# Optimization experiments

Measured on AMD Instinct MI355X. Metric: run time of the kernel, lower is better.

The kernel has to match this reference:

```python
import jax, jax.numpy as jnp
import numpy as np

D_MODEL, D_STATE, HEAD_DIM, EXPAND, K, N_GROUPS = 1024, 128, 64, 2, 4, 1
D_INNER = EXPAND * D_MODEL            # 2048
N_HEADS = D_INNER // HEAD_DIM         # 32
D_PROJ = 2 * D_INNER + 2 * N_GROUPS * D_STATE + N_HEADS  # 4384
EPS = 1e-6


def setup_inputs() -> dict:
    key = jax.random.key(0)
    ks = jax.random.split(key, 8)
    B, L = 2, 2048
    x = jax.random.normal(ks[0], (B, L, D_MODEL), dtype=jnp.float32)
    norm_w = jnp.ones((D_MODEL,), jnp.float32)
    in_proj_w = jax.random.normal(ks[1], (D_PROJ, D_MODEL), jnp.float32) * (D_MODEL ** -0.5)
    conv_w = jax.random.normal(ks[2], (D_INNER, 1, K), jnp.float32) * (K ** -0.5)
    conv_b = jnp.zeros((D_INNER,), jnp.float32)
    A_log = jnp.log(jax.random.uniform(ks[3], (N_HEADS,)) * 15.0 + 1.0)
    D = jnp.ones((N_HEADS,), jnp.float32)
    dt_bias = jnp.log(jax.random.uniform(ks[4], (N_HEADS,)) * 0.099 + 0.001)
    out_proj_w = jax.random.normal(ks[5], (D_MODEL, D_INNER), jnp.float32) * (D_INNER ** -0.5)
    return {"x": x, "norm_w": norm_w, "in_proj_w": in_proj_w, "conv_w": conv_w,
            "conv_b": conv_b, "A_log": A_log, "D": D, "dt_bias": dt_bias,
            "out_proj_w": out_proj_w}


def _silu(v):
    return v * jax.nn.sigmoid(v)


def reference(x, norm_w, in_proj_w, conv_w, conv_b, A_log, D, dt_bias, out_proj_w):
    Bsz, L, _ = x.shape
    residual = x
    # RMSNorm (pre-norm)
    xn = x * jax.lax.rsqrt(jnp.mean(x * x, axis=-1, keepdims=True) + EPS) * norm_w
    proj = xn @ in_proj_w.T                                     # (B, L, D_PROJ)
    # split fused projection -> (z, x_ssm, B, C, dt_raw)
    i = 0
    z = proj[..., i:i + D_INNER]; i += D_INNER
    x_ssm = proj[..., i:i + D_INNER]; i += D_INNER
    bc = N_GROUPS * D_STATE
    Bm = proj[..., i:i + bc].reshape(Bsz, L, N_GROUPS, D_STATE); i += bc
    Cm = proj[..., i:i + bc].reshape(Bsz, L, N_GROUPS, D_STATE); i += bc
    dt_raw = proj[..., i:i + N_HEADS]
    # causal depthwise conv1d (torch pad=K-1 then slice [:L] == left-pad K-1)
    xc = jnp.transpose(x_ssm, (0, 2, 1))                        # (B, D_INNER, L)
    xc = jax.lax.conv_general_dilated(
        xc, conv_w, window_strides=(1,), padding=[(K - 1, 0)],
        dimension_numbers=("NCH", "OIH", "NCH"), feature_group_count=D_INNER)
    xc = xc + conv_b[None, :, None]
    x_conv = _silu(jnp.transpose(xc, (0, 2, 1)))                # (B, L, D_INNER)
    # discretisation
    dt = jax.nn.softplus(dt_raw + dt_bias)                      # (B, L, H)
    dA = jnp.exp(-jnp.exp(A_log)[None, None, :] * dt)           # (B, L, H)
    x_heads = x_conv.reshape(Bsz, L, N_HEADS, HEAD_DIM)
    dt_x = dt[..., None] * x_heads                              # (B, L, H, P)
    group_idx = jnp.arange(N_HEADS) // (N_HEADS // N_GROUPS)
    Bg = Bm[:, :, group_idx, :]                                 # (B, L, H, N)
    Cg = Cm[:, :, group_idx, :]
    # sequential selective scan over time via lax.scan (fp32 state)
    def step(h, inp):
        dA_t, dtx_t, B_t, C_t = inp                             # (B,H),(B,H,P),(B,H,N),(B,H,N)
        h = h * dA_t[..., None, None] + dtx_t[..., None] * B_t[:, :, None, :]
        y_t = jnp.einsum("bhpn,bhn->bhp", h, C_t)
        return h, y_t
    h0 = jnp.zeros((Bsz, N_HEADS, HEAD_DIM, D_STATE), jnp.float32)
    xs = (jnp.moveaxis(dA, 1, 0).astype(jnp.float32),
          jnp.moveaxis(dt_x, 1, 0).astype(jnp.float32),
          jnp.moveaxis(Bg, 1, 0).astype(jnp.float32),
          jnp.moveaxis(Cg, 1, 0).astype(jnp.float32))
    _, y = jax.lax.scan(step, h0, xs)                           # y: (L, B, H, P)
    y = jnp.moveaxis(y, 0, 1).astype(x.dtype)                   # (B, L, H, P)
    y = y + D[None, None, :, None] * x_heads
    y = y.reshape(Bsz, L, D_INNER) * _silu(z)                   # gated output
    return residual + y @ out_proj_w.T
```

## Files before the change

kernel.cpp:

```cpp
#include <hip/hip_runtime.h>
#include <math.h>

#define B_SZ     2
#define L_SEQ    2048
#define DM       1024
#define DP       4384
#define PS       4480
#define DI       2048
#define NH       32
#define HD       64
#define DS       128
#define M_ROWS   (B_SZ * L_SEQ)
#define QCH      64
#define NC       (L_SEQ / QCH)

typedef __bf16 bf16x8 __attribute__((ext_vector_type(8)));
typedef __bf16 bf16x4 __attribute__((ext_vector_type(4)));
typedef __bf16 bf16x2 __attribute__((ext_vector_type(2)));
typedef float  f32x4  __attribute__((ext_vector_type(4)));

__device__ __forceinline__ void gload16(const void* g, void* l) {
    __builtin_amdgcn_global_load_lds(
        (const __attribute__((address_space(1))) unsigned int*)g,
        (__attribute__((address_space(3))) unsigned int*)l,
        16, 0, 0);
}

__global__ __launch_bounds__(256) void k_prep(const float* __restrict__ Wp,
                                              __bf16* __restrict__ Wpb,
                                              const float* __restrict__ x,
                                              const float* __restrict__ w,
                                              __bf16* __restrict__ xn) {
    int tid = threadIdx.x;
    if (blockIdx.x < 4384) {
        int i = blockIdx.x * 256 + tid;
        float4 v = ((const float4*)Wp)[i];
        bf16x4 o = { (__bf16)v.x, (__bf16)v.y, (__bf16)v.z, (__bf16)v.w };
        ((bf16x4*)Wpb)[i] = o;
        return;
    }
    int row = blockIdx.x - 4384;
    const float4* x4 = (const float4*)(x + (long)row * DM);
    float4 v = x4[tid];
    float ss = v.x * v.x + v.y * v.y + v.z * v.z + v.w * v.w;
    #pragma unroll
    for (int off = 32; off > 0; off >>= 1) ss += __shfl_xor(ss, off, 64);
    __shared__ float sred[4];
    if ((tid & 63) == 0) sred[tid >> 6] = ss;
    __syncthreads();
    float tot = sred[0] + sred[1] + sred[2] + sred[3];
    float scale = rsqrtf(tot * (1.0f / (float)DM) + 1e-6f);
    const float4* w4 = (const float4*)w;
    float4 wv = w4[tid];
    bf16x4 o = { (__bf16)(v.x * scale * wv.x), (__bf16)(v.y * scale * wv.y),
                 (__bf16)(v.z * scale * wv.z), (__bf16)(v.w * scale * wv.w) };
    ((bf16x4*)(xn + (long)row * DM))[tid] = o;
}

__global__ __launch_bounds__(256) void k_gemm_bf(const __bf16* __restrict__ A,
                                                 const __bf16* __restrict__ W,
                                                 __bf16* __restrict__ Cb,
                                                 float* __restrict__ Dt,
                                                 int Nw, int K, int ldc) {
    __shared__ __align__(16) __bf16 As[2][128 * 64];
    __shared__ __align__(16) __bf16 Bs[2][128 * 64];
    int t = threadIdx.x;

    int gx = gridDim.x;
    int nwg = gx * gridDim.y;
    int orig = blockIdx.y * gx + blockIdx.x;
    int wgid = (nwg & 7) ? orig : ((orig & 7) * (nwg >> 3) + (orig >> 3));
    int bx = wgid % gx, by = wgid / gx;
    int bm = by * 128, bn = bx * 128;

    int lane = t & 63, w = t >> 6;

    int rl = lane >> 3;
    int lc = (lane & 7) ^ rl;
    int rbase = w * 32 + rl;
    const __bf16* Agp[4];
    const __bf16* Wgp[4];
    #pragma unroll
    for (int i = 0; i < 4; i++) {
        Agp[i] = A + (long)(bm + rbase + i * 8) * K + lc * 8;
        int rb = bn + rbase + i * 8; if (rb >= Nw) rb = Nw - 1;
        Wgp[i] = W + (long)rb * K + lc * 8;
    }

    int wm = (w & 1) * 64, wn = (w >> 1) * 64;
    int ln = lane & 15;
    int q  = lane >> 4;

    f32x4 acc[4][4] = {};

    int nst = K >> 6;

    #pragma unroll
    for (int i = 0; i < 4; i++) {
        gload16(Agp[i], As[0] + (w * 4 + i) * 512);
        gload16(Wgp[i], Bs[0] + (w * 4 + i) * 512);
    }

    int cur = 0;
    for (int s = 0; s < nst; ++s) {
        if (s + 1 < nst) {
            long k1 = (long)(s + 1) << 6;
            #pragma unroll
            for (int i = 0; i < 4; i++) {
                gload16(Agp[i] + k1, As[cur ^ 1] + (w * 4 + i) * 512);
                gload16(Wgp[i] + k1, Bs[cur ^ 1] + (w * 4 + i) * 512);
            }
            asm volatile("s_waitcnt vmcnt(8)" ::: "memory");
        } else {
            asm volatile("s_waitcnt vmcnt(0)" ::: "memory");
        }
        __builtin_amdgcn_sched_barrier(0);
        __builtin_amdgcn_s_barrier();
        __builtin_amdgcn_sched_barrier(0);
        __builtin_amdgcn_s_setprio(1);

        const __bf16* Asc = As[cur];
        const __bf16* Bsc = Bs[cur];
        #pragma unroll
        for (int h = 0; h < 2; h++) {
            int ch = (4 * h + q);
            int koff = ((ch ^ (ln & 7)) << 3);
            bf16x8 af[4], bfr[4];
            #pragma unroll
            for (int i = 0; i < 4; i++)
                af[i]  = *(const bf16x8*)(Asc + (wm + ln + i * 16) * 64 + koff);
            #pragma unroll
            for (int j = 0; j < 4; j++)
                bfr[j] = *(const bf16x8*)(Bsc + (wn + ln + j * 16) * 64 + koff);
            #pragma unroll
            for (int i = 0; i < 4; i++)
                #pragma unroll
                for (int j = 0; j < 4; j++)
                    acc[i][j] = __builtin_amdgcn_mfma_f32_16x16x32_bf16(
                                    af[i], bfr[j], acc[i][j], 0, 0, 0);
        }
        __builtin_amdgcn_s_setprio(0);
        __builtin_amdgcn_sched_barrier(0);
        __builtin_amdgcn_s_barrier();
        __builtin_amdgcn_sched_barrier(0);
        cur ^= 1;
    }

    int colbase = bn + wn + ln;
    #pragma unroll
    for (int i = 0; i < 4; i++) {
        #pragma unroll
        for (int r = 0; r < 4; r++) {
            int m = bm + wm + i * 16 + (lane >> 4) * 4 + r;
            long off = (long)m * ldc + colbase;
            #pragma unroll
            for (int j = 0; j < 4; j++) {
                float v = acc[i][j][r];
                Cb[off + j * 16] = (__bf16)v;
                int col = colbase + j * 16;
                if (col >= 4352 && col < 4384)
                    Dt[(long)m * 32 + (col - 4352)] = v;
            }
        }
    }
}

__global__ __launch_bounds__(256) void k_gemm_out(const __bf16* __restrict__ A,
                                                  const __bf16* __restrict__ W,
                                                  const float* __restrict__ resid,
                                                  float* __restrict__ Cf,
                                                  int K, int ldc) {
    __shared__ __align__(16) __bf16 As[2][64 * 64];
    __shared__ __align__(16) __bf16 Bs[2][128 * 64];
    int t = threadIdx.x;

    int gx = gridDim.x;
    int nwg = gx * gridDim.y;
    int orig = blockIdx.y * gx + blockIdx.x;
    int wgid = (nwg & 7) ? orig : ((orig & 7) * (nwg >> 3) + (orig >> 3));
    int bx = wgid % gx, by = wgid / gx;
    int bm = by * 64, bn = bx * 128;

    int lane = t & 63, w = t >> 6;

    int rl = lane >> 3;
    int lc = (lane & 7) ^ rl;
    const __bf16* Agp[2];
    const __bf16* Wgp[4];
    #pragma unroll
    for (int i = 0; i < 2; i++)
        Agp[i] = A + (long)(bm + w * 16 + i * 8 + rl) * K + lc * 8;
    #pragma unroll
    for (int i = 0; i < 4; i++)
        Wgp[i] = W + (long)(bn + w * 32 + i * 8 + rl) * K + lc * 8;

    int wm = (w & 1) * 32, wn = (w >> 1) * 64;
    int ln = lane & 15;
    int q  = lane >> 4;

    f32x4 acc[2][4] = {};

    int nst = K >> 6;

    #pragma unroll
    for (int i = 0; i < 2; i++) gload16(Agp[i], As[0] + (w * 2 + i) * 512);
    #pragma unroll
    for (int i = 0; i < 4; i++) gload16(Wgp[i], Bs[0] + (w * 4 + i) * 512);

    int cur = 0;
    for (int s = 0; s < nst; ++s) {
        if (s + 1 < nst) {
            long k1 = (long)(s + 1) << 6;
            #pragma unroll
            for (int i = 0; i < 2; i++)
                gload16(Agp[i] + k1, As[cur ^ 1] + (w * 2 + i) * 512);
            #pragma unroll
            for (int i = 0; i < 4; i++)
                gload16(Wgp[i] + k1, Bs[cur ^ 1] + (w * 4 + i) * 512);
            asm volatile("s_waitcnt vmcnt(6)" ::: "memory");
        } else {
            asm volatile("s_waitcnt vmcnt(0)" ::: "memory");
        }
        __builtin_amdgcn_sched_barrier(0);
        __builtin_amdgcn_s_barrier();
        __builtin_amdgcn_sched_barrier(0);
        __builtin_amdgcn_s_setprio(1);

        const __bf16* Asc = As[cur];
        const __bf16* Bsc = Bs[cur];
        #pragma unroll
        for (int h = 0; h < 2; h++) {
            int ch = (4 * h + q);
            int koff = ((ch ^ (ln & 7)) << 3);
            bf16x8 af[2], bfr[4];
            #pragma unroll
            for (int i = 0; i < 2; i++)
                af[i]  = *(const bf16x8*)(Asc + (wm + ln + i * 16) * 64 + koff);
            #pragma unroll
            for (int j = 0; j < 4; j++)
                bfr[j] = *(const bf16x8*)(Bsc + (wn + ln + j * 16) * 64 + koff);
            #pragma unroll
            for (int i = 0; i < 2; i++)
                #pragma unroll
                for (int j = 0; j < 4; j++)
                    acc[i][j] = __builtin_amdgcn_mfma_f32_16x16x32_bf16(
                                    af[i], bfr[j], acc[i][j], 0, 0, 0);
        }
        __builtin_amdgcn_s_setprio(0);
        __builtin_amdgcn_sched_barrier(0);
        __builtin_amdgcn_s_barrier();
        __builtin_amdgcn_sched_barrier(0);
        cur ^= 1;
    }

    int colbase = bn + wn + ln;
    #pragma unroll
    for (int i = 0; i < 2; i++) {
        #pragma unroll
        for (int r = 0; r < 4; r++) {
            int m = bm + wm + i * 16 + (lane >> 4) * 4 + r;
            long off = (long)m * ldc + colbase;
            #pragma unroll
            for (int j = 0; j < 4; j++) {
                float v = acc[i][j][r] + resid[off + j * 16];
                Cf[off + j * 16] = v;
            }
        }
    }
}

__global__ __launch_bounds__(256) void k_chunk(const __bf16* __restrict__ projb,
                                               const float* __restrict__ dtraw,
                                               const float* __restrict__ cw,
                                               const float* __restrict__ cb,
                                               const float* __restrict__ A_log,
                                               const float* __restrict__ dt_bias,
                                               const float* __restrict__ Dv,
                                               float* __restrict__ clog,
                                               __bf16* __restrict__ yssm,
                                               __bf16* __restrict__ Sloc) {
    int blk = blockIdx.x;
    int c  = blk & 31;
    int hh = (blk >> 5) & 31;
    int b  = blk >> 10;
    int tid = threadIdx.x;
    long rowbase = (long)b * L_SEQ + c * QCH;

    __shared__ __align__(16) __bf16 sB[64 * 136];
    __shared__ __align__(16) __bf16 sU[128 * 72];
    __shared__ __align__(16) __bf16 sXT[64 * 72];
    __shared__ __align__(16) __bf16 sXCM[67 * 72];
    __shared__ __align__(16) __bf16 sXCo[64 * 72];
    __shared__ float sCW[256];
    __shared__ float sCB[64];
    __shared__ float sclog[64];
    __shared__ float sdt[64];
    __shared__ float sw[64];

    #pragma unroll
    for (int j = 0; j < 4; j++) {
        int off = j * 256 + tid;
        int t  = off >> 4;
        int n8 = (off & 15) * 8;
        const __bf16* pr = projb + (rowbase + t) * (long)PS;
        *(bf16x8*)&sB[t * 136 + n8] = *(const bf16x8*)(pr + 4096 + n8);
        *(bf16x8*)&sU[t * 136 + n8] = *(const bf16x8*)(pr + 4224 + n8);
    }
    #pragma unroll
    for (int j = 0; j < 3; j++) {
        int off = j * 256 + tid;
        if (off < 536) {
            int ss = off >> 3;
            int p8 = (off & 7) * 8;
            bf16x8 xv;
            #pragma unroll
            for (int k = 0; k < 8; k++) xv[k] = (__bf16)0.0f;
            if (c > 0 || ss >= 3)
                xv = *(const bf16x8*)(projb + (rowbase + ss - 3) * (long)PS + DI + hh * HD + p8);
            *(bf16x8*)&sXCM[ss * 72 + p8] = xv;
        }
    }
    sCW[tid] = cw[hh * 256 + tid];
    if (tid < 64) sCB[tid] = cb[hh * 64 + tid];

    if (tid < 64) {
        float xr = dtraw[(rowbase + tid) * 32 + hh] + dt_bias[hh];
        float dt = (xr > 20.0f) ? xr : log1pf(expf(xr));
        float la = -expf(A_log[hh]);
        float v = la * dt;
        #pragma unroll
        for (int off = 1; off < 64; off <<= 1) {
            float u = __shfl_up(v, off, 64);
            if (tid >= off) v += u;
        }
        sdt[tid] = dt;
        sclog[tid] = v;
        clog[(rowbase + tid) * NH + hh] = v;
    }
    __syncthreads();

    {
        int p8 = (tid & 7) * 8;
        float wreg[8][4], breg[8];
        #pragma unroll
        for (int e = 0; e < 8; e++) {
            breg[e] = sCB[p8 + e];
            #pragma unroll
            for (int j = 0; j < 4; j++) wreg[e][j] = sCW[(p8 + e) * 4 + j];
        }
        #pragma unroll
        for (int i = 0; i < 2; i++) {
            int s = i * 32 + (tid >> 3);
            bf16x8 r0 = *(const bf16x8*)&sXCM[(s + 0) * 72 + p8];
            bf16x8 r1 = *(const bf16x8*)&sXCM[(s + 1) * 72 + p8];
            bf16x8 r2 = *(const bf16x8*)&sXCM[(s + 2) * 72 + p8];
            bf16x8 r3 = *(const bf16x8*)&sXCM[(s + 3) * 72 + p8];
            float dts = sdt[s];
            bf16x8 oc;
            #pragma unroll
            for (int e = 0; e < 8; e++) {
                float acc = breg[e];
                acc = fmaf(wreg[e][0], (float)r0[e], acc);
                acc = fmaf(wreg[e][1], (float)r1[e], acc);
                acc = fmaf(wreg[e][2], (float)r2[e], acc);
                acc = fmaf(wreg[e][3], (float)r3[e], acc);
                float xc = acc / (1.0f + expf(-acc));
                oc[e] = (__bf16)xc;
                sXT[(p8 + e) * 72 + s] = (__bf16)(dts * xc);
            }
            *(bf16x8*)&sXCo[s * 72 + p8] = oc;
        }
    }
    if (tid < 64) sw[tid] = expf(sclog[63] - sclog[tid]);
    __syncthreads();

    int lane = tid & 63, w = tid >> 6;
    int ln = lane & 15;
    int quad = lane >> 4;
    int kc = quad * 8;

    bf16x8 caf[4];
    #pragma unroll
    for (int k0 = 0; k0 < 4; k0++)
        caf[k0] = *(const bf16x8*)&sU[(16 * w + ln) * 136 + kc + k0 * 32];
    f32x4 g[4] = {};
    #pragma unroll
    for (int j = 0; j < 4; j++)
        #pragma unroll
        for (int k0 = 0; k0 < 4; k0++) {
            bf16x8 bf_ = *(const bf16x8*)&sB[(16 * j + ln) * 136 + kc + k0 * 32];
            g[j] = __builtin_amdgcn_mfma_f32_16x16x32_bf16(caf[k0], bf_, g[j], 0, 0, 0);
        }

    {
        int trow = 16 * w + quad * 4;
        #pragma unroll
        for (int r = 0; r < 4; r++) {
            int t = trow + r;
            float ct = sclog[t];
            #pragma unroll
            for (int j = 0; j < 4; j++) {
                int s = 16 * j + ln;
                float v = (s <= t) ? g[j][r] * expf(ct - sclog[s]) : 0.0f;
                sXCM[t * 72 + s] = (__bf16)v;
            }
        }
    }
    __syncthreads();

    #pragma unroll
    for (int j = 0; j < 4; j++) {
        int s  = tid & 63;
        int n8 = (j * 4 + (tid >> 6)) * 8;
        bf16x8 v = *(const bf16x8*)&sB[s * 136 + n8];
        #pragma unroll
        for (int k = 0; k < 8; k++) sU[(n8 + k) * 72 + s] = v[k];
    }

    {
        float Dh = Dv[hh];
        bf16x8 maf[2];
        #pragma unroll
        for (int k0 = 0; k0 < 2; k0++)
            maf[k0] = *(const bf16x8*)&sXCM[(16 * w + ln) * 72 + kc + k0 * 32];
        f32x4 y[4] = {};
        #pragma unroll
        for (int j = 0; j < 4; j++)
            #pragma unroll
            for (int k0 = 0; k0 < 2; k0++) {
                bf16x8 xf = *(const bf16x8*)&sXT[(16 * j + ln) * 72 + kc + k0 * 32];
                y[j] = __builtin_amdgcn_mfma_f32_16x16x32_bf16(maf[k0], xf, y[j], 0, 0, 0);
            }
        #pragma unroll
        for (int j = 0; j < 4; j++)
            #pragma unroll
            for (int r = 0; r < 4; r++) {
                int t = 16 * w + quad * 4 + r;
                int p = 16 * j + ln;
                float v = y[j][r] + Dh * (float)sXCo[t * 72 + p];
                yssm[(rowbase + t) * DI + hh * HD + p] = (__bf16)v;
            }
    }
    __syncthreads();

    {
        bf16x8 xaf[2];
        #pragma unroll
        for (int k0 = 0; k0 < 2; k0++) {
            bf16x8 raw = *(const bf16x8*)&sXT[(16 * w + ln) * 72 + kc + k0 * 32];
            bf16x8 sc;
            #pragma unroll
            for (int jj = 0; jj < 8; jj++) {
                int s = kc + k0 * 32 + jj;
                sc[jj] = (__bf16)((float)raw[jj] * sw[s]);
            }
            xaf[k0] = sc;
        }
        f32x4 sacc[8] = {};
        #pragma unroll
        for (int j = 0; j < 8; j++)
            #pragma unroll
            for (int k0 = 0; k0 < 2; k0++) {
                bf16x8 btf = *(const bf16x8*)&sU[(16 * j + ln) * 72 + kc + k0 * 32];
                sacc[j] = __builtin_amdgcn_mfma_f32_16x16x32_bf16(xaf[k0], btf, sacc[j], 0, 0, 0);
            }
        long sbase = ((long)(b * NH + hh) * NC + c) * (HD * DS);
        #pragma unroll
        for (int j = 0; j < 8; j++)
            #pragma unroll
            for (int r = 0; r < 4; r++) {
                int p = 16 * w + quad * 4 + r;
                int n = 16 * j + ln;
                Sloc[sbase + p * DS + n] = (__bf16)sacc[j][r];
            }
    }
}

__global__ __launch_bounds__(256) void k_carry_f2b(__bf16* __restrict__ Sloc,
                                                   const float* __restrict__ clog,
                                                   const float* __restrict__ Wo,
                                                   __bf16* __restrict__ Wob) {
    int bid = blockIdx.x;
    int tid = threadIdx.x;
    if (bid >= 1024) {
        int i = (bid - 1024) * 256 + tid;
        float4 v = ((const float4*)Wo)[i];
        bf16x4 o = { (__bf16)v.x, (__bf16)v.y, (__bf16)v.z, (__bf16)v.w };
        ((bf16x4*)Wob)[i] = o;
        return;
    }
    int idx = bid * 256 + tid;
    int n2 = idx & 63;
    int p  = (idx >> 6) & 63;
    int hh = (idx >> 12) & 31;
    int b  = idx >> 17;
    long base = ((long)(b * NH + hh) * NC) * (HD * DS) + p * DS + n2 * 2;
    float T0 = 0.0f, T1 = 0.0f;
    for (int c = 0; c < NC; c++) {
        float lam = expf(clog[((long)b * L_SEQ + c * QCH + QCH - 1) * NH + hh]);
        long a = base + (long)c * (HD * DS);
        bf16x2 Sv = *(const bf16x2*)&Sloc[a];
        float S0 = (float)Sv[0], S1 = (float)Sv[1];
        bf16x2 Tv = { (__bf16)T0, (__bf16)T1 };
        *(bf16x2*)&Sloc[a] = Tv;
        T0 = fmaf(T0, lam, S0);
        T1 = fmaf(T1, lam, S1);
    }
}

__global__ __launch_bounds__(256, 2) void k_fix(const __bf16* __restrict__ projb,
                                                const __bf16* __restrict__ Sloc,
                                                const float* __restrict__ clog,
                                                const __bf16* __restrict__ yb,
                                                __bf16* __restrict__ yg) {
    int blk = blockIdx.x;
    int c  = blk & 31;
    int hh = (blk >> 5) & 31;
    int b  = blk >> 10;

    __shared__ __align__(16) __bf16 sC[64 * 136];
    __shared__ __align__(16) __bf16 sH[64 * 136];
    __shared__ float sP[64];

    int tid = threadIdx.x;
    long hbase = ((long)(b * NH + hh) * NC + c) * (HD * DS);
    long rowbase = (long)b * L_SEQ + c * QCH;

    #pragma unroll
    for (int j = 0; j < 4; j++) {
        int off = j * 256 + tid;
        int t  = off >> 4;
        int n8 = (off & 15) * 8;
        *(bf16x8*)&sC[t * 136 + n8] =
            *(const bf16x8*)(projb + (rowbase + t) * (long)PS + 4224 + n8);
    }
    #pragma unroll
    for (int j = 0; j < 4; j++) {
        int off = j * 256 + tid;
        int p  = off >> 4;
        int n8 = (off & 15) * 8;
        *(bf16x8*)&sH[p * 136 + n8] = *(const bf16x8*)&Sloc[hbase + (long)off * 8];
    }
    if (tid < 64) sP[tid] = expf(clog[(rowbase + tid) * NH + hh]);
    __syncthreads();

    int lane = tid & 63, w = tid >> 6;
    int ln = lane & 15;
    int quad = lane >> 4;
    int kc = quad * 8;

    bf16x8 caf[4];
    #pragma unroll
    for (int k0 = 0; k0 < 4; k0++)
        caf[k0] = *(const bf16x8*)&sC[(16 * w + ln) * 136 + kc + k0 * 32];
    f32x4 acc4[4] = {};
    #pragma unroll
    for (int j = 0; j < 4; j++)
        #pragma unroll
        for (int k0 = 0; k0 < 4; k0++) {
            bf16x8 hf = *(const bf16x8*)&sH[(16 * j + ln) * 136 + kc + k0 * 32];
            acc4[j] = __builtin_amdgcn_mfma_f32_16x16x32_bf16(caf[k0], hf, acc4[j], 0, 0, 0);
        }

    #pragma unroll
    for (int j = 0; j < 4; j++)
        #pragma unroll
        for (int r = 0; r < 4; r++) {
            int t = 16 * w + quad * 4 + r;
            int p = 16 * j + ln;
            long row = rowbase + t;
            long yoff = row * DI + hh * HD + p;
            float pm = sP[t];
            float z = (float)projb[row * (long)PS + hh * HD + p];
            float o = ((float)yb[yoff] + pm * acc4[j][r]) * (z / (1.0f + expf(-z)));
            yg[yoff] = (__bf16)o;
        }
}

extern "C" void kernel_launch(void* const* d_in, const int* in_sizes, int n_in,
                              void* d_out, int out_size, void* d_ws, size_t ws_size,
                              hipStream_t stream) {
    const float* x       = (const float*)d_in[0];
    const float* norm_w  = (const float*)d_in[1];
    const float* Wp      = (const float*)d_in[2];
    const float* cw      = (const float*)d_in[3];
    const float* cb      = (const float*)d_in[4];
    const float* A_log   = (const float*)d_in[5];
    const float* Dv      = (const float*)d_in[6];
    const float* dt_bias = (const float*)d_in[7];
    const float* Wo      = (const float*)d_in[8];
    float* out = (float*)d_out;

    float* ws     = (float*)d_ws;
    __bf16* projb = (__bf16*)ws;
    float* dtraw  = ws    + 9175040;
    float* clog   = dtraw + 131072;
    float* ybh    = clog  + 131072;
    float* ybf    = ybh   + 4194304;
    float* wob_s  = ybf   + 4194304;
    float* U      = wob_s + 1048576;

    __bf16* xnb  = (__bf16*)U;
    __bf16* Wpb  = (__bf16*)(U + 2097152);
    __bf16* Sloc = (__bf16*)U;
    __bf16* Wob  = (__bf16*)wob_s;
    __bf16* ybb  = (__bf16*)ybf;
    __bf16* yb   = (__bf16*)ybh;

    k_prep<<<4384 + M_ROWS, 256, 0, stream>>>(Wp, Wpb, x, norm_w, xnb);
    {
        dim3 g(PS / 128, M_ROWS / 128);
        k_gemm_bf<<<g, 256, 0, stream>>>(xnb, Wpb, projb, dtraw, DP, DM, PS);
    }

    k_chunk<<<B_SZ * NH * NC, 256, 0, stream>>>(projb, dtraw, cw, cb, A_log,
                                                dt_bias, Dv, clog, yb, Sloc);
    k_carry_f2b<<<3072, 256, 0, stream>>>(Sloc, clog, Wo, Wob);
    k_fix<<<B_SZ * NH * NC, 256, 0, stream>>>(projb, Sloc, clog, yb, ybb);

    {
        dim3 g(DM / 128, M_ROWS / 64);
        k_gemm_out<<<g, 256, 0, stream>>>(ybb, Wob, x, out, DI, DM);
    }
}
```

Measured before the change: 261.1 us.

## Restructure input projection GEMM into 256x128 tiles with triple-buffered split prefetch

The input-projection GEMM now uses 512-thread blocks covering 256x128 output tiles, with eight waves in a 4x2 layout. LDS goes from double to triple buffering, loading two stages ahead. Each k-step's global-to-LDS loads are split into two halves interleaved with the two MFMA half-steps. The aim is to hide memory latency better and reuse the weight tile across more rows. In exchange it uses more LDS per block (about 144KB) and launches half as many blocks, which may reduce occupancy and wave coverage on the CUs.

```diff
diff --git a/kernel.cpp b/kernel.cpp
--- a/kernel.cpp
+++ b/kernel.cpp
@@ -57,13 +57,13 @@
     ((bf16x4*)(xn + (long)row * DM))[tid] = o;
 }
 
-__global__ __launch_bounds__(256) void k_gemm_bf(const __bf16* __restrict__ A,
+__global__ __launch_bounds__(512) void k_gemm_in(const __bf16* __restrict__ A,
                                                  const __bf16* __restrict__ W,
                                                  __bf16* __restrict__ Cb,
                                                  float* __restrict__ Dt,
                                                  int Nw, int K, int ldc) {
-    __shared__ __align__(16) __bf16 As[2][128 * 64];
-    __shared__ __align__(16) __bf16 Bs[2][128 * 64];
+    __shared__ __align__(16) __bf16 As[3][256 * 64];
+    __shared__ __align__(16) __bf16 Bs[3][128 * 64];
     int t = threadIdx.x;
 
     int gx = gridDim.x;
@@ -71,23 +71,25 @@
     int orig = blockIdx.y * gx + blockIdx.x;
     int wgid = (nwg & 7) ? orig : ((orig & 7) * (nwg >> 3) + (orig >> 3));
     int bx = wgid % gx, by = wgid / gx;
-    int bm = by * 128, bn = bx * 128;
+    int bm = by * 256, bn = bx * 128;
 
     int lane = t & 63, w = t >> 6;
 
     int rl = lane >> 3;
     int lc = (lane & 7) ^ rl;
-    int rbase = w * 32 + rl;
     const __bf16* Agp[4];
-    const __bf16* Wgp[4];
-    #pragma unroll
-    for (int i = 0; i < 4; i++) {
-        Agp[i] = A + (long)(bm + rbase + i * 8) * K + lc * 8;
-        int rb = bn + rbase + i * 8; if (rb >= Nw) rb = Nw - 1;
+    #pragma unroll
+    for (int i = 0; i < 4; i++)
+        Agp[i] = A + (long)(bm + w * 32 + i * 8 + rl) * K + lc * 8;
+    const __bf16* Wgp[2];
+    #pragma unroll
+    for (int i = 0; i < 2; i++) {
+        int rb = bn + w * 16 + i * 8 + rl; if (rb >= Nw) rb = Nw - 1;
         Wgp[i] = W + (long)rb * K + lc * 8;
     }
 
-    int wm = (w & 1) * 64, wn = (w >> 1) * 64;
+    int wr = w >> 1, wc = w & 1;
+    int wm = wr * 64, wn = wc * 64;
     int ln = lane & 15;
     int q  = lane >> 4;
 
@@ -96,35 +98,35 @@
     int nst = K >> 6;
 
     #pragma unroll
-    for (int i = 0; i < 4; i++) {
-        gload16(Agp[i], As[0] + (w * 4 + i) * 512);
-        gload16(Wgp[i], Bs[0] + (w * 4 + i) * 512);
-    }
+    for (int p = 0; p < 2; ++p) {
+        long kk = (long)p << 6;
+        #pragma unroll
+        for (int i = 0; i < 4; i++) gload16(Agp[i] + kk, As[p] + (w * 4 + i) * 512);
+        #pragma unroll
+        for (int i = 0; i < 2; i++) gload16(Wgp[i] + kk, Bs[p] + (w * 2 + i) * 512);
+    }
+    asm volatile("s_waitcnt vmcnt(6)" ::: "memory");
+    __builtin_amdgcn_sched_barrier(0);
+    __builtin_amdgcn_s_barrier();
+    __builtin_amdgcn_sched_barrier(0);
 
     int cur = 0;
     for (int s = 0; s < nst; ++s) {
-        if (s + 1 < nst) {
-            long k1 = (long)(s + 1) << 6;
-            #pragma unroll
-            for (int i = 0; i < 4; i++) {
-                gload16(Agp[i] + k1, As[cur ^ 1] + (w * 4 + i) * 512);
-                gload16(Wgp[i] + k1, Bs[cur ^ 1] + (w * 4 + i) * 512);
-            }
-            asm volatile("s_waitcnt vmcnt(8)" ::: "memory");
-        } else {
-            asm volatile("s_waitcnt vmcnt(0)" ::: "memory");
-        }
-        __builtin_amdgcn_sched_barrier(0);
-        __builtin_amdgcn_s_barrier();
-        __builtin_amdgcn_sched_barrier(0);
-        __builtin_amdgcn_s_setprio(1);
-
         const __bf16* Asc = As[cur];
         const __bf16* Bsc = Bs[cur];
-        #pragma unroll
-        for (int h = 0; h < 2; h++) {
-            int ch = (4 * h + q);
-            int koff = ((ch ^ (ln & 7)) << 3);
+        int nx2 = cur + 2; if (nx2 >= 3) nx2 -= 3;
+        bool pre = (s + 2 < nst);
+        long k2 = (long)(s + 2) << 6;
+        __bf16* Ad = As[nx2];
+        __bf16* Bd = Bs[nx2];
+
+        if (pre) {
+            gload16(Agp[0] + k2, Ad + (w * 4 + 0) * 512);
+            gload16(Agp[1] + k2, Ad + (w * 4 + 1) * 512);
+            gload16(Agp[2] + k2, Ad + (w * 4 + 2) * 512);
+        }
+        {
+            int koff = ((q ^ (ln & 7)) << 3);
             bf16x8 af[4], bfr[4];
             #pragma unroll
             for (int i = 0; i < 4; i++)
@@ -132,18 +134,49 @@
             #pragma unroll
             for (int j = 0; j < 4; j++)
                 bfr[j] = *(const bf16x8*)(Bsc + (wn + ln + j * 16) * 64 + koff);
+            __builtin_amdgcn_s_setprio(1);
             #pragma unroll
             for (int i = 0; i < 4; i++)
                 #pragma unroll
                 for (int j = 0; j < 4; j++)
                     acc[i][j] = __builtin_amdgcn_mfma_f32_16x16x32_bf16(
                                     af[i], bfr[j], acc[i][j], 0, 0, 0);
-        }
-        __builtin_amdgcn_s_setprio(0);
+            __builtin_amdgcn_s_setprio(0);
+        }
         __builtin_amdgcn_sched_barrier(0);
         __builtin_amdgcn_s_barrier();
         __builtin_amdgcn_sched_barrier(0);
-        cur ^= 1;
+
+        if (pre) {
+            gload16(Agp[3] + k2, Ad + (w * 4 + 3) * 512);
+            gload16(Wgp[0] + k2, Bd + (w * 2 + 0) * 512);
+            gload16(Wgp[1] + k2, Bd + (w * 2 + 1) * 512);
+        }
+        {
+            int koff = (((4 + q) ^ (ln & 7)) << 3);
+            bf16x8 af[4], bfr[4];
+            #pragma unroll
+            for (int i = 0; i < 4; i++)
+                af[i]  = *(const bf16x8*)(Asc + (wm + ln + i * 16) * 64 + koff);
+            #pragma unroll
+            for (int j = 0; j < 4; j++)
+                bfr[j] = *(const bf16x8*)(Bsc + (wn + ln + j * 16) * 64 + koff);
+            __builtin_amdgcn_s_setprio(1);
+            #pragma unroll
+            for (int i = 0; i < 4; i++)
+                #pragma unroll
+                for (int j = 0; j < 4; j++)
+                    acc[i][j] = __builtin_amdgcn_mfma_f32_16x16x32_bf16(
+                                    af[i], bfr[j], acc[i][j], 0, 0, 0);
+            __builtin_amdgcn_s_setprio(0);
+        }
+        if (pre) asm volatile("s_waitcnt vmcnt(6)" ::: "memory");
+        else     asm volatile("s_waitcnt vmcnt(0)" ::: "memory");
+        __builtin_amdgcn_sched_barrier(0);
+        __builtin_amdgcn_s_barrier();
+        __builtin_amdgcn_sched_barrier(0);
+
+        cur = cur + 1; if (cur >= 3) cur -= 3;
     }
 
     int colbase = bn + wn + ln;
@@ -151,7 +184,7 @@
     for (int i = 0; i < 4; i++) {
         #pragma unroll
         for (int r = 0; r < 4; r++) {
-            int m = bm + wm + i * 16 + (lane >> 4) * 4 + r;
+            int m = bm + wm + i * 16 + q * 4 + r;
             long off = (long)m * ldc + colbase;
             #pragma unroll
             for (int j = 0; j < 4; j++) {
@@ -609,8 +642,8 @@
 
     k_prep<<<4384 + M_ROWS, 256, 0, stream>>>(Wp, Wpb, x, norm_w, xnb);
     {
-        dim3 g(PS / 128, M_ROWS / 128);
-        k_gemm_bf<<<g, 256, 0, stream>>>(xnb, Wpb, projb, dtraw, DP, DM, PS);
+        dim3 g(PS / 128, M_ROWS / 256);
+        k_gemm_in<<<g, 512, 0, stream>>>(xnb, Wpb, projb, dtraw, DP, DM, PS);
     }
 
     k_chunk<<<B_SZ * NH * NC, 256, 0, stream>>>(projb, dtraw, cw, cb, A_log,
```

Result: slower. 288.3 us (+10.4%).
